# Performance work log

Measured on AMD Instinct MI355X. Metric: run time of the kernel, lower is better.

## Reference

```python
import jax, jax.numpy as jnp
import numpy as np

B, C, H, W = 8, 64, 64, 64
OUT = 256
N_PAIRS = C * (C + 1) // 2          # 2080 upper-triangular (incl diag) products
N_IN = C + N_PAIRS                  # 2144 conv input channels


def setup_inputs() -> dict:
    key = jax.random.key(0)
    k1, k2 = jax.random.split(key)
    x = jax.random.normal(k1, (B, C, H, W), dtype=jnp.float32)
    fc_w = jax.random.normal(k2, (OUT, N_IN), dtype=jnp.float32) * 0.02
    return {"x": x, "fc_w": fc_w}


def reference(x, fc_w):
    # Upper-triangular indices (row-major, incl diagonal) == get_square_indices(C)
    ii, jj = np.triu_indices(x.shape[1])
    # Per-pixel outer product restricted to the needed triangular terms.
    quad = x[:, ii] * x[:, jj]                  # [B, C(C+1)/2, H, W]
    y = jnp.concatenate([x, quad], axis=1)      # [B, C(C+3)/2, H, W]
    # 1x1 conv, bias=False -> pointwise channel GEMM
    return jnp.einsum('bchw,oc->bohw', y, fc_w)
```

## Files before the change

kernel.cpp:

```cpp
#include <hip/hip_runtime.h>

using u16 = unsigned short;
using u32 = unsigned int;

typedef __attribute__((ext_vector_type(8)))  short s16x8;
typedef __attribute__((ext_vector_type(4)))  float f32x4;
typedef __attribute__((ext_vector_type(16))) float f32x16;
typedef __attribute__((ext_vector_type(4)))  u32   u32x4;

#define NQ  74
#define NQQ 72
#define WG_U16   (NQ * 8192)
#define RUNPK_OFF (WG_U16 * 2)

__device__ __forceinline__ u16 f2bf_rne(float f) {
    u32 u = __builtin_bit_cast(u32, f);
    u32 r = u + 0x7fffu + ((u >> 16) & 1u);
    return (u16)(r >> 16);
}
__device__ __forceinline__ float bf2f(u16 u) {
    u32 v = ((u32)u) << 16;
    return __builtin_bit_cast(float, v);
}

__device__ __forceinline__ void cm_decode(int r, int& i, int& j0) {
    if (r >= 288) { i = 64; j0 = (r - 288) * 8; return; }
    int c = r >> 2;
    int jr = 0;
    while (jr < 7 && (jr + 1) * (jr + 2) <= c) ++jr;
    i  = 4 * (c - jr * (jr + 1)) + (r & 3);
    j0 = 8 * jr;
}

__global__ __launch_bounds__(1024)
void pack_w(const float* __restrict__ fcw, u16* __restrict__ wg,
            u32* __restrict__ runpk) {
    const u32 g = blockIdx.x * 1024 + threadIdx.x;
    if (blockIdx.x == 0 && threadIdx.x < NQQ) {
        int q = threadIdx.x, jr = 0;
        while (jr < 7 && (jr + 1) * (jr + 2) <= q) ++jr;
        runpk[q] = ((u32)(8 * jr) << 8) | (u32)(4 * (q - jr * (jr + 1)));
    }
    const int e  = g & 7;
    const int l  = (g >> 3) & 63;
    const int kh = l >> 5;
    const int ni = (g >> 9) & 1, s = (g >> 10) & 1;
    const int nc = (g >> 11) & 1, nb = (g >> 12) & 1;
    const int q  = g >> 13;
    int i, j0; cm_decode(q * 4 + 2 * s + kh, i, j0);
    const int n = nb * 128 + nc * 64 + ni * 32 + (l & 31);
    const int j = j0 + e;
    float w;
    if (i == 64)    w = fcw[n * 2144 + j];
    else if (j < i) w = 0.f;
    else            w = fcw[n * 2144 + 64 + i * 64 - ((i * (i - 1)) >> 1) + (j - i)];
    wg[g] = f2bf_rne(w);
}

__device__ __forceinline__ s16x8 packmul(float fi, s16x8 vj) {
    u32 pk[4];
    #pragma unroll
    for (int d = 0; d < 4; ++d) {
        float p0 = fi * bf2f((u16)vj[2 * d]);
        float p1 = fi * bf2f((u16)vj[2 * d + 1]);
        pk[d] = __builtin_amdgcn_perm(__builtin_bit_cast(u32, p1),
                                      __builtin_bit_cast(u32, p0), 0x07060302u);
    }
    u32x4 pv = { pk[0], pk[1], pk[2], pk[3] };
    return __builtin_bit_cast(s16x8, pv);
}

__global__ __launch_bounds__(256, 2)
void quad_gemm(const float* __restrict__ x, const u16* __restrict__ wg,
               const u32* __restrict__ runpk, float* __restrict__ out) {
    __shared__ __align__(16) u16 xl[128 * 64];

    const int t  = threadIdx.x;
    const int l  = t & 63;
    const int wv = t >> 6;
    const int mrow = wv >> 1, nc = wv & 1;
    const int lm = l & 31, kh = l >> 5;
    const int sw = (lm & 7) << 3;

    const int mtile = (int)blockIdx.x >> 1;
    const int nb    = blockIdx.x & 1;
    const int pix0  = mtile * 128;
    const int b     = pix0 >> 12;
    const int hw0   = pix0 & 4095;

    {
        const int mg = (t & 31) * 4;
        const int cg = (t >> 5) * 8;
        const float* xp = x + ((size_t)b << 18) + (size_t)cg * 4096 + hw0 + mg;
        f32x4 vv[8];
        #pragma unroll
        for (int e = 0; e < 8; ++e)
            vv[e] = *(const f32x4*)(xp + (size_t)e * 4096);
        #pragma unroll
        for (int r = 0; r < 4; ++r) {
            u32 w4[4];
            #pragma unroll
            for (int d = 0; d < 4; ++d)
                w4[d] = (u32)f2bf_rne(vv[2 * d][r]) |
                        ((u32)f2bf_rne(vv[2 * d + 1][r]) << 16);
            int m = mg + r;
            u32x4 pv = { w4[0], w4[1], w4[2], w4[3] };
            *(u32x4*)(xl + m * 64 + (cg ^ ((m & 7) << 3))) = pv;
        }
    }

    const int pxb = mrow * 64 + lm;
    const u16* wp = wg + (size_t)(nb * 2 + nc) * 2048 + (size_t)l * 8;

    f32x16 acc[2][2];
    #pragma unroll
    for (int mi = 0; mi < 2; ++mi)
        #pragma unroll
        for (int ni = 0; ni < 2; ++ni)
            #pragma unroll
            for (int r = 0; r < 16; ++r) acc[mi][ni][r] = 0.f;

    #define LOADW(Q, W) do {                                                 \
        const u32x4* p_ = (const u32x4*)(wp + (size_t)(Q) * 8192);           \
        W[0] = p_[0]; W[1] = p_[64]; W[2] = p_[128]; W[3] = p_[192];         \
    } while (0)

    #define GENQ(Q, Y) do {                                                  \
        if ((Q) < NQQ) {                                                     \
            u32 meta_ = runpk[(Q)];                                          \
            int j0_ = (int)((meta_ >> 8) & 255u), ib_ = (int)(meta_ & 255u); \
            _Pragma("unroll")                                                \
            for (int mi_ = 0; mi_ < 2; ++mi_) {                              \
                int base_ = (pxb + mi_ * 32) * 64;                           \
                s16x8 vj_ = *(const s16x8*)(xl + base_ + (j0_ ^ sw));        \
                float f0_ = bf2f(xl[base_ + ((ib_ + kh) ^ sw)]);             \
                float f1_ = bf2f(xl[base_ + ((ib_ + 2 + kh) ^ sw)]);         \
                Y[mi_ * 2 + 0] = packmul(f0_, vj_);                          \
                Y[mi_ * 2 + 1] = packmul(f1_, vj_);                          \
            }                                                                \
        } else {                                                             \
            int cb_ = ((Q) - NQQ) * 32;                                      \
            _Pragma("unroll")                                                \
            for (int mi_ = 0; mi_ < 2; ++mi_) {                              \
                int base_ = (pxb + mi_ * 32) * 64;                           \
                _Pragma("unroll")                                            \
                for (int s_ = 0; s_ < 2; ++s_) {                             \
                    int j0_ = cb_ + 8 * (2 * s_ + kh);                       \
                    Y[mi_ * 2 + s_] =                                        \
                        *(const s16x8*)(xl + base_ + (j0_ ^ sw));            \
                }                                                            \
            }                                                                \
        }                                                                    \
    } while (0)

    #define MFMAQ(W, Y) do {                                                 \
        _Pragma("unroll")                                                    \
        for (int s_ = 0; s_ < 2; ++s_)                                       \
            _Pragma("unroll")                                                \
            for (int mi_ = 0; mi_ < 2; ++mi_)                                \
                _Pragma("unroll")                                            \
                for (int ni_ = 0; ni_ < 2; ++ni_)                            \
                    acc[mi_][ni_] = __builtin_amdgcn_mfma_f32_32x32x16_bf16( \
                        __builtin_bit_cast(s16x8, W[s_ * 2 + ni_]),          \
                        Y[mi_ * 2 + s_],                                     \
                        acc[mi_][ni_], 0, 0, 0);                             \
    } while (0)

    u32x4 Wa[4], Wb[4];
    s16x8 Ya[4], Yb[4];

    LOADW(0, Wa);
    __syncthreads();
    GENQ(0, Ya);

    #pragma unroll 1
    for (int q = 0; q + 2 < NQ; q += 2) {
        LOADW(q + 1, Wb);
        GENQ(q + 1, Yb);
        MFMAQ(Wa, Ya);
        LOADW(q + 2, Wa);
        GENQ(q + 2, Ya);
        MFMAQ(Wb, Yb);
    }
    LOADW(NQ - 1, Wb);
    GENQ(NQ - 1, Yb);
    MFMAQ(Wa, Ya);
    MFMAQ(Wb, Yb);

    float* ob = out + ((size_t)b << 20) + (size_t)hw0;
    #pragma unroll
    for (int mi = 0; mi < 2; ++mi) {
        const int px = pxb + mi * 32;
        #pragma unroll
        for (int ni = 0; ni < 2; ++ni) {
            #pragma unroll
            for (int r = 0; r < 16; ++r) {
                const int o = nb * 128 + nc * 64 + ni * 32 +
                              (r & 3) + 8 * (r >> 2) + 4 * kh;
                ob[(size_t)o * 4096 + px] = acc[mi][ni][r];
            }
        }
    }
}

extern "C" void kernel_launch(void* const* d_in, const int* in_sizes, int n_in,
                              void* d_out, int out_size, void* d_ws, size_t ws_size,
                              hipStream_t stream) {
    const float* x   = (const float*)d_in[0];
    const float* fcw = (const float*)d_in[1];
    float* out = (float*)d_out;
    u16* wg    = (u16*)d_ws;
    u32* runpk = (u32*)((char*)d_ws + RUNPK_OFF);

    hipLaunchKernelGGL(pack_w, dim3(WG_U16 / 1024), dim3(1024), 0, stream,
                       fcw, wg, runpk);
    hipLaunchKernelGGL(quad_gemm, dim3(512), dim3(256), 0, stream,
                       x, wg, runpk, out);
}
```

Baseline: 114.7 us.

## Deepen weight prefetch to four stages and add transposed LDS copy for scalar reads

Replaces the two-stage weight register double-buffer with a four-deep rotation, so global weight loads are issued three steps ahead of their MFMA use. It also adds a channel-major transposed bf16 copy of the x tile in LDS, so the per-pixel scalar factor reads become contiguous across lanes rather than strided and bank-conflicting. Run metadata is cached in LDS instead of being read from global memory. The cost is more VGPRs for the extra weight buffers, which could hurt occupancy at launch bounds (256,2), plus extra LDS for the transposed tile.

```diff
diff --git a/kernel.cpp b/kernel.cpp
--- a/kernel.cpp
+++ b/kernel.cpp
@@ -7,6 +7,7 @@
 typedef __attribute__((ext_vector_type(4)))  float f32x4;
 typedef __attribute__((ext_vector_type(16))) float f32x16;
 typedef __attribute__((ext_vector_type(4)))  u32   u32x4;
+typedef __attribute__((ext_vector_type(4)))  short s16x4;
 
 #define NQ  74
 #define NQQ 72
@@ -74,6 +75,8 @@
 void quad_gemm(const float* __restrict__ x, const u16* __restrict__ wg,
                const u32* __restrict__ runpk, float* __restrict__ out) {
     __shared__ __align__(16) u16 xl[128 * 64];
+    __shared__ __align__(16) u16 x_t[64 * 128];
+    __shared__ u32 runl[NQQ];
 
     const int t  = threadIdx.x;
     const int l  = t & 63;
@@ -88,6 +91,8 @@
     const int b     = pix0 >> 12;
     const int hw0   = pix0 & 4095;
 
+    if (t < NQQ) runl[t] = runpk[t];
+
     {
         const int mg = (t & 31) * 4;
         const int cg = (t >> 5) * 8;
@@ -96,16 +101,25 @@
         #pragma unroll
         for (int e = 0; e < 8; ++e)
             vv[e] = *(const f32x4*)(xp + (size_t)e * 4096);
+        u16 tb[8][4];
+        #pragma unroll
+        for (int e = 0; e < 8; ++e)
+            #pragma unroll
+            for (int r = 0; r < 4; ++r) tb[e][r] = f2bf_rne(vv[e][r]);
         #pragma unroll
         for (int r = 0; r < 4; ++r) {
-            u32 w4[4];
-            #pragma unroll
-            for (int d = 0; d < 4; ++d)
-                w4[d] = (u32)f2bf_rne(vv[2 * d][r]) |
-                        ((u32)f2bf_rne(vv[2 * d + 1][r]) << 16);
             int m = mg + r;
-            u32x4 pv = { w4[0], w4[1], w4[2], w4[3] };
+            u32x4 pv = { (u32)tb[0][r] | ((u32)tb[1][r] << 16),
+                         (u32)tb[2][r] | ((u32)tb[3][r] << 16),
+                         (u32)tb[4][r] | ((u32)tb[5][r] << 16),
+                         (u32)tb[6][r] | ((u32)tb[7][r] << 16) };
             *(u32x4*)(xl + m * 64 + (cg ^ ((m & 7) << 3))) = pv;
+        }
+        #pragma unroll
+        for (int e = 0; e < 8; ++e) {
+            s16x4 pv = { (short)tb[e][0], (short)tb[e][1],
+                         (short)tb[e][2], (short)tb[e][3] };
+            *(s16x4*)(x_t + ((cg + e) << 7) + mg) = pv;
         }
     }
 
@@ -121,20 +135,21 @@
             for (int r = 0; r < 16; ++r) acc[mi][ni][r] = 0.f;
 
     #define LOADW(Q, W) do {                                                 \
-        const u32x4* p_ = (const u32x4*)(wp + (size_t)(Q) * 8192);           \
+        int qc_ = (Q) < NQ ? (Q) : (NQ - 1);                                 \
+        const u32x4* p_ = (const u32x4*)(wp + (size_t)qc_ * 8192);           \
         W[0] = p_[0]; W[1] = p_[64]; W[2] = p_[128]; W[3] = p_[192];         \
     } while (0)
 
     #define GENQ(Q, Y) do {                                                  \
         if ((Q) < NQQ) {                                                     \
-            u32 meta_ = runpk[(Q)];                                          \
+            u32 meta_ = runl[(Q)];                                           \
             int j0_ = (int)((meta_ >> 8) & 255u), ib_ = (int)(meta_ & 255u); \
             _Pragma("unroll")                                                \
             for (int mi_ = 0; mi_ < 2; ++mi_) {                              \
-                int base_ = (pxb + mi_ * 32) * 64;                           \
-                s16x8 vj_ = *(const s16x8*)(xl + base_ + (j0_ ^ sw));        \
-                float f0_ = bf2f(xl[base_ + ((ib_ + kh) ^ sw)]);             \
-                float f1_ = bf2f(xl[base_ + ((ib_ + 2 + kh) ^ sw)]);         \
+                int px_ = pxb + mi_ * 32;                                    \
+                s16x8 vj_ = *(const s16x8*)(xl + (px_ << 6) + (j0_ ^ sw));   \
+                float f0_ = bf2f(x_t[((ib_ + kh) << 7) + px_]);              \
+                float f1_ = bf2f(x_t[((ib_ + 2 + kh) << 7) + px_]);          \
                 Y[mi_ * 2 + 0] = packmul(f0_, vj_);                          \
                 Y[mi_ * 2 + 1] = packmul(f1_, vj_);                          \
             }                                                                \
@@ -142,7 +157,7 @@
             int cb_ = ((Q) - NQQ) * 32;                                      \
             _Pragma("unroll")                                                \
             for (int mi_ = 0; mi_ < 2; ++mi_) {                              \
-                int base_ = (pxb + mi_ * 32) * 64;                           \
+                int base_ = (pxb + mi_ * 32) << 6;                           \
                 _Pragma("unroll")                                            \
                 for (int s_ = 0; s_ < 2; ++s_) {                             \
                     int j0_ = cb_ + 8 * (2 * s_ + kh);                       \
@@ -166,26 +181,23 @@
                         acc[mi_][ni_], 0, 0, 0);                             \
     } while (0)
 
-    u32x4 Wa[4], Wb[4];
+    u32x4 W0[4], W1[4], W2[4], W3[4];
     s16x8 Ya[4], Yb[4];
 
-    LOADW(0, Wa);
+    LOADW(0, W0); LOADW(1, W1); LOADW(2, W2); LOADW(3, W3);
     __syncthreads();
     GENQ(0, Ya);
 
     #pragma unroll 1
-    for (int q = 0; q + 2 < NQ; q += 2) {
-        LOADW(q + 1, Wb);
-        GENQ(q + 1, Yb);
-        MFMAQ(Wa, Ya);
-        LOADW(q + 2, Wa);
-        GENQ(q + 2, Ya);
-        MFMAQ(Wb, Yb);
-    }
-    LOADW(NQ - 1, Wb);
-    GENQ(NQ - 1, Yb);
-    MFMAQ(Wa, Ya);
-    MFMAQ(Wb, Yb);
+    for (int q = 0; q < 72; q += 4) {
+        GENQ(q + 1, Yb); MFMAQ(W0, Ya); LOADW(q + 4, W0);
+        GENQ(q + 2, Ya); MFMAQ(W1, Yb); LOADW(q + 5, W1);
+        GENQ(q + 3, Yb); MFMAQ(W2, Ya); LOADW(q + 6, W2);
+        GENQ(q + 4, Ya); MFMAQ(W3, Yb); LOADW(q + 7, W3);
+    }
+    GENQ(73, Yb);
+    MFMAQ(W0, Ya);
+    MFMAQ(W1, Yb);
 
     float* ob = out + ((size_t)b << 20) + (size_t)hw0;
     #pragma unroll
```

New measurement: 113.3 us. About the same (-1.2%).

## Use 1024-thread blocks covering all outputs with LDS-staged double-buffered weights

Applied to the files above, without the earlier changes.

Each block now handles a 128-pixel tile across all 256 output channels with 16 waves, instead of splitting the output channels across two blocks. This halves the grid and removes the redundant per-pixel quadratic feature generation. Weight tiles are streamed into double-buffered LDS with global_load_lds and shared by all waves, guarded by explicit waitcnt and barriers, replacing per-wave direct global loads. Each wave now covers one 32-pixel row instead of two, which cuts register pressure but adds barrier synchronisation every stage and runs only 256 blocks.

```diff
diff --git a/kernel.cpp b/kernel.cpp
--- a/kernel.cpp
+++ b/kernel.cpp
@@ -7,6 +7,7 @@
 typedef __attribute__((ext_vector_type(4)))  float f32x4;
 typedef __attribute__((ext_vector_type(16))) float f32x16;
 typedef __attribute__((ext_vector_type(4)))  u32   u32x4;
+typedef __attribute__((ext_vector_type(2)))  u32   u32x2;
 
 #define NQ  74
 #define NQQ 72
@@ -41,14 +42,14 @@
         while (jr < 7 && (jr + 1) * (jr + 2) <= q) ++jr;
         runpk[q] = ((u32)(8 * jr) << 8) | (u32)(4 * (q - jr * (jr + 1)));
     }
-    const int e  = g & 7;
-    const int l  = (g >> 3) & 63;
-    const int kh = l >> 5;
-    const int ni = (g >> 9) & 1, s = (g >> 10) & 1;
-    const int nc = (g >> 11) & 1, nb = (g >> 12) & 1;
-    const int q  = g >> 13;
+    const int e   = g & 7;
+    const int l   = (g >> 3) & 63;
+    const int kh  = l >> 5;
+    const int ni  = (g >> 9) & 1, s = (g >> 10) & 1;
+    const int nc2 = (g >> 11) & 3;
+    const int q   = g >> 13;
     int i, j0; cm_decode(q * 4 + 2 * s + kh, i, j0);
-    const int n = nb * 128 + nc * 64 + ni * 32 + (l & 31);
+    const int n = nc2 * 64 + ni * 32 + (l & 31);
     const int j = j0 + e;
     float w;
     if (i == 64)    w = fcw[n * 2144 + j];
@@ -70,85 +71,74 @@
     return __builtin_bit_cast(s16x8, pv);
 }
 
-__global__ __launch_bounds__(256, 2)
+__global__ __launch_bounds__(1024, 4)
 void quad_gemm(const float* __restrict__ x, const u16* __restrict__ wg,
                const u32* __restrict__ runpk, float* __restrict__ out) {
     __shared__ __align__(16) u16 xl[128 * 64];
-
-    const int t  = threadIdx.x;
-    const int l  = t & 63;
-    const int wv = t >> 6;
-    const int mrow = wv >> 1, nc = wv & 1;
-    const int lm = l & 31, kh = l >> 5;
-    const int sw = (lm & 7) << 3;
-
-    const int mtile = (int)blockIdx.x >> 1;
-    const int nb    = blockIdx.x & 1;
-    const int pix0  = mtile * 128;
-    const int b     = pix0 >> 12;
-    const int hw0   = pix0 & 4095;
+    __shared__ __align__(16) u16 wbuf[2][8192];
+    __shared__ u32 runl[NQQ];
+
+    const int t   = threadIdx.x;
+    const int l   = t & 63;
+    const int wv  = t >> 6;
+    const int mrow = wv >> 2, nc2 = wv & 3;
+    const int lm  = l & 31, kh = l >> 5;
+    const int sw  = (lm & 7) << 3;
+
+    const int pix0 = (int)blockIdx.x * 128;
+    const int b    = pix0 >> 12;
+    const int hw0  = pix0 & 4095;
+
+    if (t < NQQ) runl[t] = runpk[t];
 
     {
         const int mg = (t & 31) * 4;
-        const int cg = (t >> 5) * 8;
-        const float* xp = x + ((size_t)b << 18) + (size_t)cg * 4096 + hw0 + mg;
-        f32x4 vv[8];
-        #pragma unroll
-        for (int e = 0; e < 8; ++e)
-            vv[e] = *(const f32x4*)(xp + (size_t)e * 4096);
+        const int cp = (t >> 5) * 2;
+        const float* xp = x + ((size_t)b << 18) + (size_t)cp * 4096 + hw0 + mg;
+        f32x4 v0 = *(const f32x4*)(xp);
+        f32x4 v1 = *(const f32x4*)(xp + 4096);
         #pragma unroll
         for (int r = 0; r < 4; ++r) {
-            u32 w4[4];
-            #pragma unroll
-            for (int d = 0; d < 4; ++d)
-                w4[d] = (u32)f2bf_rne(vv[2 * d][r]) |
-                        ((u32)f2bf_rne(vv[2 * d + 1][r]) << 16);
             int m = mg + r;
-            u32x4 pv = { w4[0], w4[1], w4[2], w4[3] };
-            *(u32x4*)(xl + m * 64 + (cg ^ ((m & 7) << 3))) = pv;
+            u32 pv = (u32)f2bf_rne(v0[r]) | ((u32)f2bf_rne(v1[r]) << 16);
+            *(u32*)(xl + m * 64 + (cp ^ ((m & 7) << 3))) = pv;
         }
     }
 
-    const int pxb = mrow * 64 + lm;
-    const u16* wp = wg + (size_t)(nb * 2 + nc) * 2048 + (size_t)l * 8;
-
-    f32x16 acc[2][2];
-    #pragma unroll
-    for (int mi = 0; mi < 2; ++mi)
-        #pragma unroll
-        for (int ni = 0; ni < 2; ++ni)
-            #pragma unroll
-            for (int r = 0; r < 16; ++r) acc[mi][ni][r] = 0.f;
-
-    #define LOADW(Q, W) do {                                                 \
-        const u32x4* p_ = (const u32x4*)(wp + (size_t)(Q) * 8192);           \
-        W[0] = p_[0]; W[1] = p_[64]; W[2] = p_[128]; W[3] = p_[192];         \
+    const int xrow  = (mrow * 32 + lm) << 6;
+    const int wboff = nc2 * 2048 + l * 8;
+    const u16* wsrc = wg + (size_t)t * 8;
+
+    #define STAGEQ(Q, DSTP) __builtin_amdgcn_global_load_lds(                \
+        (const __attribute__((address_space(1))) void*)(wsrc + (size_t)(Q) * 8192), \
+        (__attribute__((address_space(3))) void*)((char*)(DSTP) + t * 16), 16, 0, 0)
+
+    #define LOADWF(SRC, W) do {                                              \
+        const u16* bp_ = (SRC) + wboff;                                      \
+        W[0] = *(const u32x4*)(bp_);                                         \
+        W[1] = *(const u32x4*)(bp_ + 512);                                   \
+        W[2] = *(const u32x4*)(bp_ + 1024);                                  \
+        W[3] = *(const u32x4*)(bp_ + 1536);                                  \
     } while (0)
 
     #define GENQ(Q, Y) do {                                                  \
         if ((Q) < NQQ) {                                                     \
-            u32 meta_ = runpk[(Q)];                                          \
+            u32 meta_ = runl[(Q)];                                           \
             int j0_ = (int)((meta_ >> 8) & 255u), ib_ = (int)(meta_ & 255u); \
+            s16x8 vj_ = *(const s16x8*)(xl + xrow + (j0_ ^ sw));             \
+            u32x2 fq_ = *(const u32x2*)(xl + xrow + (ib_ ^ sw));             \
             _Pragma("unroll")                                                \
-            for (int mi_ = 0; mi_ < 2; ++mi_) {                              \
-                int base_ = (pxb + mi_ * 32) * 64;                           \
-                s16x8 vj_ = *(const s16x8*)(xl + base_ + (j0_ ^ sw));        \
-                float f0_ = bf2f(xl[base_ + ((ib_ + kh) ^ sw)]);             \
-                float f1_ = bf2f(xl[base_ + ((ib_ + 2 + kh) ^ sw)]);         \
-                Y[mi_ * 2 + 0] = packmul(f0_, vj_);                          \
-                Y[mi_ * 2 + 1] = packmul(f1_, vj_);                          \
+            for (int s_ = 0; s_ < 2; ++s_) {                                 \
+                u32 fw_ = fq_[s_];                                           \
+                u32 fb_ = kh ? (fw_ & 0xffff0000u) : (fw_ << 16);            \
+                Y[s_] = packmul(__builtin_bit_cast(float, fb_), vj_);        \
             }                                                                \
         } else {                                                             \
             int cb_ = ((Q) - NQQ) * 32;                                      \
             _Pragma("unroll")                                                \
-            for (int mi_ = 0; mi_ < 2; ++mi_) {                              \
-                int base_ = (pxb + mi_ * 32) * 64;                           \
-                _Pragma("unroll")                                            \
-                for (int s_ = 0; s_ < 2; ++s_) {                             \
-                    int j0_ = cb_ + 8 * (2 * s_ + kh);                       \
-                    Y[mi_ * 2 + s_] =                                        \
-                        *(const s16x8*)(xl + base_ + (j0_ ^ sw));            \
-                }                                                            \
+            for (int s_ = 0; s_ < 2; ++s_) {                                 \
+                int j0_ = cb_ + 8 * (2 * s_ + kh);                           \
+                Y[s_] = *(const s16x8*)(xl + xrow + (j0_ ^ sw));             \
             }                                                                \
         }                                                                    \
     } while (0)
@@ -157,48 +147,65 @@
         _Pragma("unroll")                                                    \
         for (int s_ = 0; s_ < 2; ++s_)                                       \
             _Pragma("unroll")                                                \
-            for (int mi_ = 0; mi_ < 2; ++mi_)                                \
-                _Pragma("unroll")                                            \
-                for (int ni_ = 0; ni_ < 2; ++ni_)                            \
-                    acc[mi_][ni_] = __builtin_amdgcn_mfma_f32_32x32x16_bf16( \
-                        __builtin_bit_cast(s16x8, W[s_ * 2 + ni_]),          \
-                        Y[mi_ * 2 + s_],                                     \
-                        acc[mi_][ni_], 0, 0, 0);                             \
+            for (int ni_ = 0; ni_ < 2; ++ni_)                                \
+                acc[ni_] = __builtin_amdgcn_mfma_f32_32x32x16_bf16(          \
+                    __builtin_bit_cast(s16x8, W[s_ * 2 + ni_]),              \
+                    Y[s_], acc[ni_], 0, 0, 0);                               \
     } while (0)
 
-    u32x4 Wa[4], Wb[4];
-    s16x8 Ya[4], Yb[4];
-
-    LOADW(0, Wa);
+    #define FENCE asm volatile("" ::: "memory")
+
+    f32x16 acc[2];
+    #pragma unroll
+    for (int ni = 0; ni < 2; ++ni)
+        #pragma unroll
+        for (int r = 0; r < 16; ++r) acc[ni][r] = 0.f;
+
+    u16* wc = &wbuf[0][0];
+    u16* wn = &wbuf[1][0];
+    u32x4 Wf[4];
+    s16x8 Ya[2], Yb[2];
+
+    STAGEQ(0, wc);
+    STAGEQ(1, wn);
     __syncthreads();
     GENQ(0, Ya);
 
     #pragma unroll 1
-    for (int q = 0; q + 2 < NQ; q += 2) {
-        LOADW(q + 1, Wb);
+    for (int q = 0; q < 72; q += 2) {
+        asm volatile("s_waitcnt vmcnt(1)" ::: "memory");
+        __builtin_amdgcn_s_barrier(); FENCE;
+        LOADWF(wc, Wf);
         GENQ(q + 1, Yb);
-        MFMAQ(Wa, Ya);
-        LOADW(q + 2, Wa);
+        MFMAQ(Wf, Ya);
+        FENCE; __builtin_amdgcn_s_barrier(); FENCE;
+        STAGEQ(q + 2, wc);
+        asm volatile("s_waitcnt vmcnt(1)" ::: "memory");
+        __builtin_amdgcn_s_barrier(); FENCE;
+        LOADWF(wn, Wf);
         GENQ(q + 2, Ya);
-        MFMAQ(Wb, Yb);
-    }
-    LOADW(NQ - 1, Wb);
-    GENQ(NQ - 1, Yb);
-    MFMAQ(Wa, Ya);
-    MFMAQ(Wb, Yb);
+        MFMAQ(Wf, Yb);
+        FENCE; __builtin_amdgcn_s_barrier(); FENCE;
+        STAGEQ(q + 3, wn);
+    }
+    asm volatile("s_waitcnt vmcnt(1)" ::: "memory");
+    __builtin_amdgcn_s_barrier(); FENCE;
+    LOADWF(wc, Wf);
+    GENQ(73, Yb);
+    MFMAQ(Wf, Ya);
+    asm volatile("s_waitcnt vmcnt(0)" ::: "memory");
+    __builtin_amdgcn_s_barrier(); FENCE;
+    LOADWF(wn, Wf);
+    MFMAQ(Wf, Yb);
 
     float* ob = out + ((size_t)b << 20) + (size_t)hw0;
+    const int px = mrow * 32 + lm;
     #pragma unroll
-    for (int mi = 0; mi < 2; ++mi) {
-        const int px = pxb + mi * 32;
+    for (int ni = 0; ni < 2; ++ni) {
         #pragma unroll
-        for (int ni = 0; ni < 2; ++ni) {
-            #pragma unroll
-            for (int r = 0; r < 16; ++r) {
-                const int o = nb * 128 + nc * 64 + ni * 32 +
-                              (r & 3) + 8 * (r >> 2) + 4 * kh;
-                ob[(size_t)o * 4096 + px] = acc[mi][ni][r];
-            }
+        for (int r = 0; r < 16; ++r) {
+            const int o = nc2 * 64 + ni * 32 + 4 * kh + (r & 3) + 8 * (r >> 2);
+            ob[(size_t)o * 4096 + px] = acc[ni][r];
         }
     }
 }
@@ -214,6 +221,6 @@
 
     hipLaunchKernelGGL(pack_w, dim3(WG_U16 / 1024), dim3(1024), 0, stream,
                        fcw, wg, runpk);
-    hipLaunchKernelGGL(quad_gemm, dim3(512), dim3(256), 0, stream,
+    hipLaunchKernelGGL(quad_gemm, dim3(256), dim3(1024), 0, stream,
                        x, wg, runpk, out);
 }
```

New measurement: 122.6 us. 6.9% more time.
